# Optimization experiments

Hardware: AMD Instinct MI355X
Metric: run time of the kernel (lower is better)

## Reference

```python
import jax, jax.numpy as jnp
import numpy as np

N = 20000
E = 320000
D = 256
OUT = 256
NEG_SLOPE = 0.2


def setup_inputs() -> dict:
    key = jax.random.key(0)
    ks = jax.random.split(key, 16)
    s = 1.0 / np.sqrt(D)
    x = jax.random.normal(ks[0], (N, D), dtype=jnp.float32)
    edge_index = jax.random.randint(ks[1], (2, E), 0, N, dtype=jnp.int64)
    W1 = jax.random.uniform(ks[2], (D, D), jnp.float32, -s, s)
    W2 = jax.random.uniform(ks[3], (D, D), jnp.float32, -s, s)
    Ws = jax.random.uniform(ks[4], (6, D, D), jnp.float32, -s, s)      # per-layer GATConv lin weight
    a_src = jax.random.uniform(ks[5], (6, D), jnp.float32, -s, s)      # per-layer att_src
    a_dst = jax.random.uniform(ks[6], (6, D), jnp.float32, -s, s)      # per-layer att_dst
    bias = jnp.zeros((6, D), dtype=jnp.float32)                        # per-layer GATConv bias
    W3 = jax.random.uniform(ks[7], (2 * D, OUT), jnp.float32, -s, s)
    return {"x": x, "edge_index": edge_index, "W1": W1, "W2": W2,
            "Ws": Ws, "a_src": a_src, "a_dst": a_dst, "bias": bias, "W3": W3}


def _gat_layer(h, src, dst, W, asrc, adst, b):
    # h: [N, D] -> linear transform
    hw = h @ W                                         # [N, D]
    e_src = hw @ asrc                                  # [N]
    e_dst = hw @ adst                                  # [N]
    e = jax.nn.leaky_relu(e_src[src] + e_dst[dst], NEG_SLOPE)  # [E]
    # softmax over incoming edges per destination node
    m = jax.ops.segment_max(e, dst, num_segments=N)    # [N], -inf for empty segs (unused)
    ee = jnp.exp(e - m[dst])                           # [E]
    denom = jax.ops.segment_sum(ee, dst, num_segments=N)
    alpha = ee / denom[dst]                            # [E]
    msg = alpha[:, None] * hw[src]                     # [E, D]
    out = jax.ops.segment_sum(msg, dst, num_segments=N)  # [N, D]
    return out + b


def reference(x, edge_index, W1, W2, Ws, a_src, a_dst, bias, W3):
    src, dst = edge_index[0], edge_index[1]
    h = x @ W1
    h = h @ W2
    for i in range(6):
        h = _gat_layer(h, src, dst, Ws[i], a_src[i], a_dst[i], bias[i])
    h = jnp.concatenate((h, h), axis=1)   # [N, 2D]
    h = jax.nn.relu(h)
    return h @ W3                          # [N, OUT]
```

## Files before the change

kernel.cpp:

```cpp
#include <hip/hip_runtime.h>
#include <hip/hip_fp16.h>
#include <stdint.h>

#define NNODES 20000
#define EEDGES 320000
#define DD     256
#define NEG_SLOPE 0.2f
#define SCAN_BLOCKS ((NNODES + 255) / 256)
#define ESTR   20480

typedef _Float16 half8 __attribute__((ext_vector_type(8)));
typedef _Float16 half4 __attribute__((ext_vector_type(4)));
typedef float f32x4 __attribute__((ext_vector_type(4)));


__global__ void zero_ints_k(int* __restrict__ p, int n) {
    int i = blockIdx.x * 256 + threadIdx.x;
    if (i < n) p[i] = 0;
}

__global__ void hist_k(const int* __restrict__ dst, int* __restrict__ rowptr) {
    int i = blockIdx.x * 256 + threadIdx.x;
    if (i < EEDGES) atomicAdd(&rowptr[dst[i] + 1], 1);
}

__global__ __launch_bounds__(256) void scan1_k(int* __restrict__ rowptr, int* __restrict__ bsums) {
    __shared__ int buf[256];
    int idx = blockIdx.x * 256 + threadIdx.x;
    int v = (idx < NNODES) ? rowptr[idx + 1] : 0;
    buf[threadIdx.x] = v;
    __syncthreads();
#pragma unroll
    for (int off = 1; off < 256; off <<= 1) {
        int t = (threadIdx.x >= (unsigned)off) ? buf[threadIdx.x - off] : 0;
        __syncthreads();
        buf[threadIdx.x] += t;
        __syncthreads();
    }
    if (idx < NNODES) rowptr[idx + 1] = buf[threadIdx.x];
    if (threadIdx.x == 255) bsums[blockIdx.x] = buf[255];
}

__global__ __launch_bounds__(128) void scan2_k(int* __restrict__ bsums) {
    __shared__ int buf[128];
    int v = (threadIdx.x < SCAN_BLOCKS) ? bsums[threadIdx.x] : 0;
    buf[threadIdx.x] = v;
    __syncthreads();
#pragma unroll
    for (int off = 1; off < 128; off <<= 1) {
        int t = (threadIdx.x >= (unsigned)off) ? buf[threadIdx.x - off] : 0;
        __syncthreads();
        buf[threadIdx.x] += t;
        __syncthreads();
    }
    if (threadIdx.x < SCAN_BLOCKS) bsums[threadIdx.x] = buf[threadIdx.x];
}

__global__ void scan3_k(int* __restrict__ rowptr, const int* __restrict__ bsums,
                        int* __restrict__ cursor) {
    int idx = blockIdx.x * 256 + threadIdx.x;
    if (idx < NNODES) {
        int v = rowptr[idx + 1];
        if (blockIdx.x > 0) { v += bsums[blockIdx.x - 1]; rowptr[idx + 1] = v; }
        if (idx + 1 < NNODES) cursor[idx + 1] = v;
        if (idx == 0) cursor[0] = 0;
    }
}

__global__ void scatter_k(const int* __restrict__ src, const int* __restrict__ dst,
                          int* __restrict__ cursor, int* __restrict__ colsrc) {
    int i = blockIdx.x * 256 + threadIdx.x;
    if (i < EEDGES) {
        int d = dst[i];
        int pos = atomicAdd(&cursor[d], 1);
        colsrc[pos] = src[i];
    }
}


__global__ void cvt_weights_k(const float* __restrict__ W1, const float* __restrict__ W2,
                              const float* __restrict__ Ws, const float* __restrict__ W3,
                              _Float16* __restrict__ WT) {
    int i = blockIdx.x * 256 + threadIdx.x;
    if (i >= DD * DD) return;
    const size_t WSZ = (size_t)DD * DD;
    int y = blockIdx.y;
    _Float16* Wh = WT + (size_t)y * 2 * WSZ;
    _Float16* Wl = Wh + WSZ;
    if (y == 0) {
        float v = W1[i];
        _Float16 hi = (_Float16)v;
        Wh[i] = hi;
        Wl[i] = (_Float16)(v - (float)hi);
    } else {
        const float* W = (y == 1) ? W2 : (y == 8) ? W3 : (Ws + (size_t)(y - 2) * WSZ);
        int k = i >> 8, n = i & 255;
        float v = W[i];
        if (y == 8) v += W3[i + WSZ];
        _Float16 hi = (_Float16)v;
        Wh[n * DD + k] = hi;
        Wl[n * DD + k] = (_Float16)(v - (float)hi);
    }
}


template<bool A_FP32, bool OUT_SPLIT, bool DOTS>
__global__ __launch_bounds__(512, 4) void gemm_k(
    const float* __restrict__ Af,
    const _Float16* __restrict__ Ah, const _Float16* __restrict__ Al,
    const _Float16* __restrict__ Bh, const _Float16* __restrict__ Bl,
    float* __restrict__ C, _Float16* __restrict__ Ch, _Float16* __restrict__ Cl,
    const float* __restrict__ asrc, const float* __restrict__ adst,
    float* __restrict__ esp, float* __restrict__ edp, int M)
{
    const int nwg = gridDim.x;
    const int orig = blockIdx.x;
    const int q = nwg >> 3, r = nwg & 7;
    const int xcd = orig & 7, idx = orig >> 3;
    const int sw = (xcd < r ? xcd * (q + 1) : r * (q + 1) + (xcd - r) * q) + idx;
    const int by = sw >> 1;
    const int bx = sw & 1;

    __shared__ _Float16 smem[24576];
    _Float16* sAh = smem;
    _Float16* sAl = smem + 4096;
    _Float16* sBh = smem + 8192;
    _Float16* sBl = smem + 16384;

    const int t = threadIdx.x;
    const int lane = t & 63;
    const int w = t >> 6;
    const int rowBase = by * 64;
    const int colBase = bx * 128;
    const int mo = (w & 1) * 32;
    const int no = (w >> 1) * 32;

    const int arow = t >> 3;
    const int slot = t & 7;
    const int swz = (slot ^ (arow & 7)) << 3;

    const int garow = (rowBase + arow < M) ? (rowBase + arow) : (M - 1);

    f32x4 acc[2][2];
#pragma unroll
    for (int m = 0; m < 2; ++m)
#pragma unroll
        for (int n = 0; n < 2; ++n) acc[m][n] = (f32x4){0.f, 0.f, 0.f, 0.f};

    int4 pa_h, pa_l, pb_h0, pb_h1, pb_l0, pb_l1;
    f32x4 fa0, fa1;

#define LOADSTAGE(S) { \
        size_t aoff  = (size_t)garow * DD + (S) * 64 + slot * 8; \
        size_t boff0 = (size_t)(colBase + arow) * DD + (S) * 64 + slot * 8; \
        size_t boff1 = boff0 + (size_t)64 * DD; \
        if constexpr (A_FP32) { \
            fa0 = *(const f32x4*)(Af + aoff); \
            fa1 = *(const f32x4*)(Af + aoff + 4); \
        } else { \
            pa_h = *(const int4*)(Ah + aoff); \
            pa_l = *(const int4*)(Al + aoff); \
        } \
        pb_h0 = *(const int4*)(Bh + boff0); \
        pb_h1 = *(const int4*)(Bh + boff1); \
        pb_l0 = *(const int4*)(Bl + boff0); \
        pb_l1 = *(const int4*)(Bl + boff1); \
    }

#define WRITESTAGE() { \
        int da  = arow * 64 + swz; \
        if constexpr (A_FP32) { \
            half8 hv, lv; \
            _Pragma("unroll") \
            for (int i = 0; i < 4; ++i) { \
                float v0 = fa0[i]; _Float16 h0 = (_Float16)v0; \
                hv[i] = h0; lv[i] = (_Float16)(v0 - (float)h0); \
                float v1 = fa1[i]; _Float16 h1 = (_Float16)v1; \
                hv[4 + i] = h1; lv[4 + i] = (_Float16)(v1 - (float)h1); \
            } \
            *(half8*)(sAh + da) = hv; \
            *(half8*)(sAl + da) = lv; \
        } else { \
            *(int4*)(sAh + da) = pa_h; \
            *(int4*)(sAl + da) = pa_l; \
        } \
        *(int4*)(sBh + da) = pb_h0; \
        *(int4*)(sBh + da + 4096) = pb_h1; \
        *(int4*)(sBl + da) = pb_l0; \
        *(int4*)(sBl + da + 4096) = pb_l1; \
    }

    LOADSTAGE(0);
    const int fr = lane & 15;
    const int fq = lane >> 4;

    for (int s = 0; s < 4; ++s) {
        __syncthreads();
        WRITESTAGE();
        __syncthreads();
        if (s < 3) { LOADSTAGE(s + 1); }

#pragma unroll
        for (int kk = 0; kk < 2; ++kk) {
            const int c = kk * 4 + fq;
            half8 ah[2], al[2], bh[2], bl[2];
#pragma unroll
            for (int m = 0; m < 2; ++m) {
                int ra = mo + m * 16 + fr;
                int oa = ra * 64 + ((c ^ (ra & 7)) << 3);
                ah[m] = *(const half8*)(sAh + oa);
                al[m] = *(const half8*)(sAl + oa);
            }
#pragma unroll
            for (int n = 0; n < 2; ++n) {
                int rb = no + n * 16 + fr;
                int ob = rb * 64 + ((c ^ (rb & 7)) << 3);
                bh[n] = *(const half8*)(sBh + ob);
                bl[n] = *(const half8*)(sBl + ob);
            }
#pragma unroll
            for (int m = 0; m < 2; ++m)
#pragma unroll
                for (int n = 0; n < 2; ++n) {
                    acc[m][n] = __builtin_amdgcn_mfma_f32_16x16x32_f16(ah[m], bh[n], acc[m][n], 0, 0, 0);
                    acc[m][n] = __builtin_amdgcn_mfma_f32_16x16x32_f16(ah[m], bl[n], acc[m][n], 0, 0, 0);
                    acc[m][n] = __builtin_amdgcn_mfma_f32_16x16x32_f16(al[m], bh[n], acc[m][n], 0, 0, 0);
                    acc[m][n] = __builtin_amdgcn_mfma_f32_16x16x32_f16(al[m], bl[n], acc[m][n], 0, 0, 0);
                }
        }
    }
#undef LOADSTAGE
#undef WRITESTAGE

    const int ccol = lane & 15;
    const int crq = (lane >> 4) * 4;

    if constexpr (OUT_SPLIT) {
        __syncthreads();
#pragma unroll
        for (int m = 0; m < 2; ++m)
#pragma unroll
            for (int n = 0; n < 2; ++n)
#pragma unroll
                for (int r = 0; r < 4; ++r) {
                    int row = mo + m * 16 + crq + r;
                    int col = no + n * 16 + ccol;
                    float v = acc[m][n][r];
                    _Float16 hi = (_Float16)v;
                    smem[row * 136 + col] = hi;
                    smem[8704 + row * 136 + col] = (_Float16)(v - (float)hi);
                }
        __syncthreads();
#pragma unroll
        for (int i = 0; i < 2; ++i) {
            int slotId = i * 512 + t;
            int srow = slotId >> 4;
            int sc = slotId & 15;
            int grow = rowBase + srow;
            if (grow < M) {
                half8 hv = *(const half8*)(smem + srow * 136 + sc * 8);
                half8 lv = *(const half8*)(smem + 8704 + srow * 136 + sc * 8);
                *(half8*)(Ch + (size_t)grow * DD + colBase + sc * 8) = hv;
                *(half8*)(Cl + (size_t)grow * DD + colBase + sc * 8) = lv;
            }
        }
    } else {
#pragma unroll
        for (int m = 0; m < 2; ++m) {
            int growb = rowBase + mo + m * 16 + crq;
#pragma unroll
            for (int n = 0; n < 2; ++n) {
                int gcol = colBase + no + n * 16 + ccol;
#pragma unroll
                for (int r = 0; r < 4; ++r) {
                    int grow = growb + r;
                    if (grow < M) C[(size_t)grow * DD + gcol] = acc[m][n][r];
                }
            }
        }
    }

    if constexpr (DOTS) {
        float as0 = asrc[colBase + no + ccol];
        float as1 = asrc[colBase + no + 16 + ccol];
        float ad0 = adst[colBase + no + ccol];
        float ad1 = adst[colBase + no + 16 + ccol];
        __syncthreads();
        float* sred = (float*)smem;
        const int cw = w >> 1;
#pragma unroll
        for (int m = 0; m < 2; ++m)
#pragma unroll
            for (int r = 0; r < 4; ++r) {
                float ps = acc[m][0][r] * as0 + acc[m][1][r] * as1;
                float pd = acc[m][0][r] * ad0 + acc[m][1][r] * ad1;
#pragma unroll
                for (int off = 1; off < 16; off <<= 1) {
                    ps += __shfl_xor(ps, off);
                    pd += __shfl_xor(pd, off);
                }
                if (ccol == 0) {
                    int row = mo + m * 16 + crq + r;
                    sred[row * 8 + cw] = ps;
                    sred[512 + row * 8 + cw] = pd;
                }
            }
        __syncthreads();
        if (t < 64) {
            float esb = sred[t * 8 + 0] + sred[t * 8 + 1] + sred[t * 8 + 2] + sred[t * 8 + 3];
            float edb = sred[512 + t * 8 + 0] + sred[512 + t * 8 + 1]
                      + sred[512 + t * 8 + 2] + sred[512 + t * 8 + 3];
            int grow = rowBase + t;
            if (grow < M) {
                esp[(size_t)bx * ESTR + grow] = esb;
                edp[(size_t)bx * ESTR + grow] = edb;
            }
        }
    }
}


template<bool RELU>
__global__ __launch_bounds__(256) void gat_agg_k(const float* __restrict__ hw,
                                                 const float* __restrict__ es0,
                                                 const float* __restrict__ es1,
                                                 const float* __restrict__ ed0,
                                                 const float* __restrict__ ed1,
                                                 const int* __restrict__ rowptr,
                                                 const int* __restrict__ colsrc,
                                                 float* __restrict__ ealpha,
                                                 const float* __restrict__ bias,
                                                 float* __restrict__ hout) {
    int wave = threadIdx.x >> 6;
    int lane = threadIdx.x & 63;
    int node = blockIdx.x * 4 + wave;
    if (node >= NNODES) return;
    int start = rowptr[node], end = rowptr[node + 1];
    int deg = end - start;
    float edd = ed0[node] + ed1[node];

    float4 acc0 = make_float4(0.f, 0.f, 0.f, 0.f);
    float4 acc1 = acc0, acc2 = acc0, acc3 = acc0;
    float4 acc4 = acc0, acc5 = acc0, acc6 = acc0, acc7 = acc0;

#define FMA4(ACC, W_, V) \
    ACC.x = fmaf(W_, V.x, ACC.x); ACC.y = fmaf(W_, V.y, ACC.y); \
    ACC.z = fmaf(W_, V.z, ACC.z); ACC.w = fmaf(W_, V.w, ACC.w);

    if (deg <= 64) {
        if (deg > 0) {
            int j = start + lane;
            bool valid = j < end;
            int msrc = valid ? colsrc[j] : 0;
            float e = valid ? es0[msrc] + es1[msrc] + edd : -INFINITY;
            e = fmaxf(e, NEG_SLOPE * e);
            float mx = e;
#pragma unroll
            for (int off = 32; off; off >>= 1) mx = fmaxf(mx, __shfl_xor(mx, off));
            float ee = valid ? expf(e - mx) : 0.f;
            float sum = ee;
#pragma unroll
            for (int off = 32; off; off >>= 1) sum += __shfl_xor(sum, off);
            float w = ee / sum;

            int j2 = 0;
            for (; j2 + 8 <= deg; j2 += 8) {
                int s0 = __shfl(msrc, j2 + 0), s1 = __shfl(msrc, j2 + 1);
                int s2 = __shfl(msrc, j2 + 2), s3 = __shfl(msrc, j2 + 3);
                int s4 = __shfl(msrc, j2 + 4), s5 = __shfl(msrc, j2 + 5);
                int s6 = __shfl(msrc, j2 + 6), s7 = __shfl(msrc, j2 + 7);
                float w0 = __shfl(w, j2 + 0), w1 = __shfl(w, j2 + 1);
                float w2 = __shfl(w, j2 + 2), w3 = __shfl(w, j2 + 3);
                float w4 = __shfl(w, j2 + 4), w5 = __shfl(w, j2 + 5);
                float w6 = __shfl(w, j2 + 6), w7 = __shfl(w, j2 + 7);
                float4 v0 = *(const float4*)(hw + (size_t)s0 * DD + lane * 4);
                float4 v1 = *(const float4*)(hw + (size_t)s1 * DD + lane * 4);
                float4 v2 = *(const float4*)(hw + (size_t)s2 * DD + lane * 4);
                float4 v3 = *(const float4*)(hw + (size_t)s3 * DD + lane * 4);
                float4 v4 = *(const float4*)(hw + (size_t)s4 * DD + lane * 4);
                float4 v5 = *(const float4*)(hw + (size_t)s5 * DD + lane * 4);
                float4 v6 = *(const float4*)(hw + (size_t)s6 * DD + lane * 4);
                float4 v7 = *(const float4*)(hw + (size_t)s7 * DD + lane * 4);
                FMA4(acc0, w0, v0); FMA4(acc1, w1, v1);
                FMA4(acc2, w2, v2); FMA4(acc3, w3, v3);
                FMA4(acc4, w4, v4); FMA4(acc5, w5, v5);
                FMA4(acc6, w6, v6); FMA4(acc7, w7, v7);
            }
            if (j2 + 4 <= deg) {
                int s0 = __shfl(msrc, j2 + 0), s1 = __shfl(msrc, j2 + 1);
                int s2 = __shfl(msrc, j2 + 2), s3 = __shfl(msrc, j2 + 3);
                float w0 = __shfl(w, j2 + 0), w1 = __shfl(w, j2 + 1);
                float w2 = __shfl(w, j2 + 2), w3 = __shfl(w, j2 + 3);
                float4 v0 = *(const float4*)(hw + (size_t)s0 * DD + lane * 4);
                float4 v1 = *(const float4*)(hw + (size_t)s1 * DD + lane * 4);
                float4 v2 = *(const float4*)(hw + (size_t)s2 * DD + lane * 4);
                float4 v3 = *(const float4*)(hw + (size_t)s3 * DD + lane * 4);
                FMA4(acc0, w0, v0); FMA4(acc1, w1, v1);
                FMA4(acc2, w2, v2); FMA4(acc3, w3, v3);
                j2 += 4;
            }
            for (; j2 < deg; ++j2) {
                int   s0 = __shfl(msrc, j2);
                float w0 = __shfl(w, j2);
                float4 v0 = *(const float4*)(hw + (size_t)s0 * DD + lane * 4);
                FMA4(acc0, w0, v0);
            }
        }
    } else {
        float mx = -INFINITY;
        for (int j = start + lane; j < end; j += 64) {
            int s = colsrc[j];
            float e = es0[s] + es1[s] + edd;
            e = fmaxf(e, NEG_SLOPE * e);
            mx = fmaxf(mx, e);
        }
#pragma unroll
        for (int off = 32; off; off >>= 1) mx = fmaxf(mx, __shfl_xor(mx, off));
        float sum = 0.f;
        for (int j = start + lane; j < end; j += 64) {
            int s = colsrc[j];
            float e = es0[s] + es1[s] + edd;
            e = fmaxf(e, NEG_SLOPE * e);
            float ee = expf(e - mx);
            ealpha[j] = ee;
            sum += ee;
        }
#pragma unroll
        for (int off = 32; off; off >>= 1) sum += __shfl_xor(sum, off);
        float inv = 1.f / sum;
        int j = start;
        for (; j + 4 <= end; j += 4) {
            int s0 = colsrc[j], s1 = colsrc[j + 1], s2 = colsrc[j + 2], s3 = colsrc[j + 3];
            float w0 = ealpha[j] * inv, w1 = ealpha[j + 1] * inv;
            float w2 = ealpha[j + 2] * inv, w3 = ealpha[j + 3] * inv;
            float4 v0 = *(const float4*)(hw + (size_t)s0 * DD + lane * 4);
            float4 v1 = *(const float4*)(hw + (size_t)s1 * DD + lane * 4);
            float4 v2 = *(const float4*)(hw + (size_t)s2 * DD + lane * 4);
            float4 v3 = *(const float4*)(hw + (size_t)s3 * DD + lane * 4);
            FMA4(acc0, w0, v0); FMA4(acc1, w1, v1);
            FMA4(acc2, w2, v2); FMA4(acc3, w3, v3);
        }
        for (; j < end; ++j) {
            int s0 = colsrc[j];
            float w0 = ealpha[j] * inv;
            float4 v0 = *(const float4*)(hw + (size_t)s0 * DD + lane * 4);
            FMA4(acc0, w0, v0);
        }
    }
#undef FMA4

    acc0.x += acc4.x; acc0.y += acc4.y; acc0.z += acc4.z; acc0.w += acc4.w;
    acc1.x += acc5.x; acc1.y += acc5.y; acc1.z += acc5.z; acc1.w += acc5.w;
    acc2.x += acc6.x; acc2.y += acc6.y; acc2.z += acc6.z; acc2.w += acc6.w;
    acc3.x += acc7.x; acc3.y += acc7.y; acc3.z += acc7.z; acc3.w += acc7.w;
    acc0.x += acc1.x; acc0.y += acc1.y; acc0.z += acc1.z; acc0.w += acc1.w;
    acc2.x += acc3.x; acc2.y += acc3.y; acc2.z += acc3.z; acc2.w += acc3.w;
    acc0.x += acc2.x; acc0.y += acc2.y; acc0.z += acc2.z; acc0.w += acc2.w;
    float4 b4 = *(const float4*)(bias + lane * 4);
    acc0.x += b4.x; acc0.y += b4.y; acc0.z += b4.z; acc0.w += b4.w;
    if (RELU) {
        acc0.x = fmaxf(acc0.x, 0.f); acc0.y = fmaxf(acc0.y, 0.f);
        acc0.z = fmaxf(acc0.z, 0.f); acc0.w = fmaxf(acc0.w, 0.f);
    }
    *(float4*)(hout + (size_t)node * DD + lane * 4) = acc0;
}


extern "C" void kernel_launch(void* const* d_in, const int* in_sizes, int n_in,
                              void* d_out, int out_size, void* d_ws, size_t ws_size,
                              hipStream_t stream) {
    const float* x     = (const float*)d_in[0];
    const int*   ei    = (const int*)d_in[1];
    const float* W1    = (const float*)d_in[2];
    const float* W2    = (const float*)d_in[3];
    const float* Ws    = (const float*)d_in[4];
    const float* a_src = (const float*)d_in[5];
    const float* a_dst = (const float*)d_in[6];
    const float* bias  = (const float*)d_in[7];
    const float* W3    = (const float*)d_in[8];
    float* out = (float*)d_out;

    const int* src = ei;
    const int* dst = ei + EEDGES;

    const size_t ND = (size_t)NNODES * DD;

    float* bufA   = (float*)d_ws;
    float* hbuf   = bufA + ND;
    float* es01   = hbuf + ND;
    float* ed01   = es01 + 2 * ESTR;
    float* ealpha = ed01 + 2 * ESTR;
    int*   rowptr = (int*)(ealpha + EEDGES);
    int*   cursor = rowptr + (NNODES + 1);
    int*   colsrc = cursor + NNODES;
    int*   bsums  = colsrc + EEDGES;
    _Float16* WT  = (_Float16*)(((uintptr_t)(bsums + SCAN_BLOCKS) + 15) & ~(uintptr_t)15);
    const size_t WSZ = (size_t)DD * DD;

#define WTH(i) (WT + (i) * 2 * WSZ)
#define WTL(i) (WT + (i) * 2 * WSZ + WSZ)

    zero_ints_k<<<(NNODES + 1 + 255) / 256, 256, 0, stream>>>(rowptr, NNODES + 1);
    hist_k<<<(EEDGES + 255) / 256, 256, 0, stream>>>(dst, rowptr);
    scan1_k<<<SCAN_BLOCKS, 256, 0, stream>>>(rowptr, bsums);
    scan2_k<<<1, 128, 0, stream>>>(bsums);
    scan3_k<<<SCAN_BLOCKS, 256, 0, stream>>>(rowptr, bsums, cursor);
    scatter_k<<<(EEDGES + 255) / 256, 256, 0, stream>>>(src, dst, cursor, colsrc);

    const int WBLK = (DD * DD + 255) / 256;
    cvt_weights_k<<<dim3(WBLK, 9), 256, 0, stream>>>(W1, W2, Ws, W3, WT);

    gemm_k<false, true, false><<<8, 512, 0, stream>>>(nullptr, WTH(1), WTL(1), WTH(0), WTL(0),
                                                      nullptr, WTH(9), WTL(9),
                                                      nullptr, nullptr, nullptr, nullptr, DD);

    const int GG = 2 * ((NNODES + 63) / 64);
    const int nodeBlocks = (NNODES + 3) / 4;

    gemm_k<true, false, false><<<GG, 512, 0, stream>>>(x, nullptr, nullptr, WTH(9), WTL(9),
                                                       hbuf, nullptr, nullptr,
                                                       nullptr, nullptr, nullptr, nullptr, NNODES);

    for (int l = 0; l < 6; ++l) {
        gemm_k<true, false, true><<<GG, 512, 0, stream>>>(hbuf, nullptr, nullptr,
                                                          WTH(2 + l), WTL(2 + l),
                                                          bufA, nullptr, nullptr,
                                                          a_src + (size_t)l * DD, a_dst + (size_t)l * DD,
                                                          es01, ed01, NNODES);
        if (l < 5)
            gat_agg_k<false><<<nodeBlocks, 256, 0, stream>>>(bufA, es01, es01 + ESTR,
                                                             ed01, ed01 + ESTR,
                                                             rowptr, colsrc, ealpha,
                                                             bias + (size_t)l * DD, hbuf);
        else
            gat_agg_k<true><<<nodeBlocks, 256, 0, stream>>>(bufA, es01, es01 + ESTR,
                                                            ed01, ed01 + ESTR,
                                                            rowptr, colsrc, ealpha,
                                                            bias + (size_t)l * DD, hbuf);
    }

    gemm_k<true, false, false><<<GG, 512, 0, stream>>>(hbuf, nullptr, nullptr, WTH(8), WTL(8),
                                                       out, nullptr, nullptr,
                                                       nullptr, nullptr, nullptr, nullptr, NNODES);
#undef WTH
#undef WTL
}
```

Measured before the change: 567.6 us.

## Load B tiles directly to LDS and drop low-low MFMA term

B-operand tiles now go straight from global memory into LDS through global_load_lds with a pre-swizzled source address, so they no longer pass through registers. The B load for each stage is issued inside the synchronised region instead of being prefetched a stage ahead. The lo*lo term of the split-fp16 product is also removed, cutting MFMA work per tile by a quarter. That term is second order and small, but precision drops a little. The B load is no longer overlapped with compute and depends on the hardware finishing the LDS write before the barrier.

```diff
diff --git a/kernel.cpp b/kernel.cpp
--- a/kernel.cpp
+++ b/kernel.cpp
@@ -12,6 +12,10 @@
 typedef _Float16 half8 __attribute__((ext_vector_type(8)));
 typedef _Float16 half4 __attribute__((ext_vector_type(4)));
 typedef float f32x4 __attribute__((ext_vector_type(4)));
+
+#define GLDS16(G, L) __builtin_amdgcn_global_load_lds( \
+    (const __attribute__((address_space(1))) unsigned int*)(const void*)(G), \
+    (__attribute__((address_space(3))) unsigned int*)(void*)(L), 16, 0, 0)
 
 
 __global__ void zero_ints_k(int* __restrict__ p, int n) {
@@ -147,13 +151,11 @@
 #pragma unroll
         for (int n = 0; n < 2; ++n) acc[m][n] = (f32x4){0.f, 0.f, 0.f, 0.f};
 
-    int4 pa_h, pa_l, pb_h0, pb_h1, pb_l0, pb_l1;
+    int4 pa_h, pa_l;
     f32x4 fa0, fa1;
 
-#define LOADSTAGE(S) { \
-        size_t aoff  = (size_t)garow * DD + (S) * 64 + slot * 8; \
-        size_t boff0 = (size_t)(colBase + arow) * DD + (S) * 64 + slot * 8; \
-        size_t boff1 = boff0 + (size_t)64 * DD; \
+#define LOADSTAGE_A(S) { \
+        size_t aoff = (size_t)garow * DD + (S) * 64 + slot * 8; \
         if constexpr (A_FP32) { \
             fa0 = *(const f32x4*)(Af + aoff); \
             fa1 = *(const f32x4*)(Af + aoff + 4); \
@@ -161,14 +163,10 @@
             pa_h = *(const int4*)(Ah + aoff); \
             pa_l = *(const int4*)(Al + aoff); \
         } \
-        pb_h0 = *(const int4*)(Bh + boff0); \
-        pb_h1 = *(const int4*)(Bh + boff1); \
-        pb_l0 = *(const int4*)(Bl + boff0); \
-        pb_l1 = *(const int4*)(Bl + boff1); \
-    }
-
-#define WRITESTAGE() { \
-        int da  = arow * 64 + swz; \
+    }
+
+#define WRITESTAGE_A() { \
+        int da = arow * 64 + swz; \
         if constexpr (A_FP32) { \
             half8 hv, lv; \
             _Pragma("unroll") \
@@ -184,21 +182,27 @@
             *(int4*)(sAh + da) = pa_h; \
             *(int4*)(sAl + da) = pa_l; \
         } \
-        *(int4*)(sBh + da) = pb_h0; \
-        *(int4*)(sBh + da + 4096) = pb_h1; \
-        *(int4*)(sBl + da) = pb_l0; \
-        *(int4*)(sBl + da + 4096) = pb_l1; \
-    }
-
-    LOADSTAGE(0);
+    }
+
+#define GLDS_B(S) { \
+        size_t bsw0 = (size_t)(colBase + arow) * DD + (S) * 64 + swz; \
+        size_t bsw1 = bsw0 + (size_t)64 * DD; \
+        GLDS16(Bh + bsw0, sBh + t * 8); \
+        GLDS16(Bh + bsw1, sBh + 4096 + t * 8); \
+        GLDS16(Bl + bsw0, sBl + t * 8); \
+        GLDS16(Bl + bsw1, sBl + 4096 + t * 8); \
+    }
+
+    LOADSTAGE_A(0);
     const int fr = lane & 15;
     const int fq = lane >> 4;
 
     for (int s = 0; s < 4; ++s) {
         __syncthreads();
-        WRITESTAGE();
-        __syncthreads();
-        if (s < 3) { LOADSTAGE(s + 1); }
+        GLDS_B(s);
+        WRITESTAGE_A();
+        __syncthreads();
+        if (s < 3) { LOADSTAGE_A(s + 1); }
 
 #pragma unroll
         for (int kk = 0; kk < 2; ++kk) {
@@ -225,12 +229,12 @@
                     acc[m][n] = __builtin_amdgcn_mfma_f32_16x16x32_f16(ah[m], bh[n], acc[m][n], 0, 0, 0);
                     acc[m][n] = __builtin_amdgcn_mfma_f32_16x16x32_f16(ah[m], bl[n], acc[m][n], 0, 0, 0);
                     acc[m][n] = __builtin_amdgcn_mfma_f32_16x16x32_f16(al[m], bh[n], acc[m][n], 0, 0, 0);
-                    acc[m][n] = __builtin_amdgcn_mfma_f32_16x16x32_f16(al[m], bl[n], acc[m][n], 0, 0, 0);
                 }
         }
     }
-#undef LOADSTAGE
-#undef WRITESTAGE
+#undef LOADSTAGE_A
+#undef WRITESTAGE_A
+#undef GLDS_B
 
     const int ccol = lane & 15;
     const int crq = (lane >> 4) * 4;
```

Measured after the change: 546.7 us. 1.04x faster.
